# Kernel optimization log

Measured on AMD Instinct MI355X. Metric: run time of the kernel, lower is better.

## Reference

```python
import jax, jax.numpy as jnp
import numpy as np

N_NODES = 100000
N_EDGES = 3200000
N_FEAT = 512
HIDDEN = 16
OUT_DIM = 1


def setup_inputs() -> dict:
    key = jax.random.key(0)
    ks = jax.random.split(key, 6)
    x = jax.random.normal(ks[0], (N_NODES, N_FEAT), dtype=jnp.float32)
    lap_vals = jax.random.uniform(ks[1], (N_EDGES,), dtype=jnp.float32)
    W1 = jax.random.normal(ks[2], (N_FEAT, HIDDEN), dtype=jnp.float32) * 0.05
    b1 = jnp.zeros((HIDDEN,), dtype=jnp.float32)
    W2 = jax.random.normal(ks[3], (HIDDEN, OUT_DIM), dtype=jnp.float32) * 0.05
    b2 = jnp.zeros((OUT_DIM,), dtype=jnp.float32)
    lap_rows = jax.random.randint(ks[4], (N_EDGES,), 0, N_NODES, dtype=jnp.int32)
    lap_cols = jax.random.randint(ks[5], (N_EDGES,), 0, N_NODES, dtype=jnp.int32)
    return {"x": x, "lap_vals": lap_vals, "W1": W1, "b1": b1,
            "W2": W2, "b2": b2, "lap_rows": lap_rows, "lap_cols": lap_cols}


def _spmm(vals, rows, cols, dense):
    # COO sparse [N,N] @ dense [N,D]: gather source rows, scale, scatter-add.
    return jax.ops.segment_sum(vals[:, None] * dense[cols], rows,
                               num_segments=N_NODES)


def reference(x, lap_vals, W1, b1, W2, b2, lap_rows, lap_cols):
    # Layer 1: dense GEMM -> sparse aggregation -> fused bias + relu
    h = jax.nn.relu(_spmm(lap_vals, lap_rows, lap_cols, x @ W1) + b1)
    # Layer 2: dense GEMM -> sparse aggregation -> fused bias + sigmoid
    out = jax.nn.sigmoid(_spmm(lap_vals, lap_rows, lap_cols, h @ W2) + b2)
    return out
```

## Files before the change

### kernel.cpp

```cpp
#include <hip/hip_runtime.h>
#include <cstdint>
#include <cstddef>

#define N_NODES 100000
#define N_EDGES 3200000
#define N_FEAT  512
#define HIDDEN  16
#define NBUCK   ((N_NODES + 127) / 128)
#define BCAP    4608
#define CHUNK   2048
#define NGB     ((N_NODES + 63) / 64)
#define NBS     ((N_EDGES + CHUNK - 1) / CHUNK)
#define AGG_T   512

static_assert(NGB == NBS, "parity interleave requires equal role counts");

__device__ __forceinline__ void gload_lds16(const float* g, void* lds) {
  __builtin_amdgcn_global_load_lds(
      (const __attribute__((address_space(1))) void*)g,
      (__attribute__((address_space(3))) void*)lds, 16, 0, 0);
}

__global__ __launch_bounds__(256)
void k_prep(int* __restrict__ cursor) {
  const int i = blockIdx.x * 256 + threadIdx.x;
  if (i < NBUCK) cursor[i] = 0;
}

__global__ __launch_bounds__(256)
void k_mega2(const float* __restrict__ x, const float* __restrict__ W1,
             float* __restrict__ xw, const int* __restrict__ rows,
             const int* __restrict__ cols, const float* __restrict__ vals,
             int* __restrict__ cursor, int2* __restrict__ binned) {
  __shared__ __align__(16) char smem[32768];
  const int t = threadIdx.x;

  if ((blockIdx.x & 1) == 0) {
    float4 (*xs)[2][256] = reinterpret_cast<float4 (*)[2][256]>(smem);
    const int l = t & 63;
    const int w = __builtin_amdgcn_readfirstlane(t >> 6);
    const int rbase = (blockIdx.x >> 1) * 64;
    const int kbase0 = w * 128;

    float acc[16];
#pragma unroll
    for (int c = 0; c < 16; ++c) acc[c] = 0.f;

    const int sq   = ((l & 3) ^ ((l >> 3) & 3)) * 4;
    const int srow = l >> 2;

    auto STAGE = [&](int b, int ck) {
      const int kb = kbase0 + ck * 16;
#pragma unroll
      for (int i = 0; i < 4; ++i) {
        int grow = rbase + i * 16 + srow;
        if (grow >= N_NODES) grow = N_NODES - 1;
        gload_lds16(x + (size_t)grow * N_FEAT + kb + sq, &xs[w][b][i * 64]);
      }
    };

    const int rsw = (l >> 1) & 3;
    auto COMPUTE = [&](int b, int ck) {
      const int kb = kbase0 + ck * 16;
#pragma unroll
      for (int q = 0; q < 4; ++q) {
        float4 xv = xs[w][b][l * 4 + (q ^ rsw)];
        float xe[4] = {xv.x, xv.y, xv.z, xv.w};
#pragma unroll
        for (int j = 0; j < 4; ++j) {
          const float* wrow = W1 + (size_t)(kb + q * 4 + j) * 16;
#pragma unroll
          for (int c = 0; c < 16; ++c)
            acc[c] = fmaf(xe[j], wrow[c], acc[c]);
        }
      }
    };

    STAGE(0, 0);
#pragma unroll 1
    for (int ck = 0; ck < 8; ++ck) {
      const int b = ck & 1;
      if (ck + 1 < 8) {
        STAGE(b ^ 1, ck + 1);
        asm volatile("s_waitcnt vmcnt(4)" ::: "memory");
      } else {
        asm volatile("s_waitcnt vmcnt(0)" ::: "memory");
      }
      COMPUTE(b, ck);
    }

    float4* red = &xs[w][0][0];
    red[l * 4 + 0] = make_float4(acc[0],  acc[1],  acc[2],  acc[3]);
    red[l * 4 + 1] = make_float4(acc[4],  acc[5],  acc[6],  acc[7]);
    red[l * 4 + 2] = make_float4(acc[8],  acc[9],  acc[10], acc[11]);
    red[l * 4 + 3] = make_float4(acc[12], acc[13], acc[14], acc[15]);
    __syncthreads();

    const int rr = t >> 2, qq = t & 3;
    const int grow = rbase + rr;
    if (grow < N_NODES) {
      const int s = rr * 4 + qq;
      float4 a = xs[0][0][s], b4 = xs[1][0][s], c4 = xs[2][0][s], d4 = xs[3][0][s];
      float4 o = make_float4(a.x + b4.x + c4.x + d4.x, a.y + b4.y + c4.y + d4.y,
                             a.z + b4.z + c4.z + d4.z, a.w + b4.w + c4.w + d4.w);
      ((float4*)xw)[(size_t)grow * 4 + qq] = o;
    }
  } else {
    int2*           stash = (int2*)smem;
    unsigned short* sbuck = (unsigned short*)(smem + 16384);
    int*            hist  = (int*)(smem + 16384 + 4096);
    int*            base  = (int*)(smem + 16384 + 4096 + 4 * NBUCK);
    const int e0 = (blockIdx.x >> 1) * CHUNK;
    const int nv = (N_EDGES - e0 < CHUNK) ? (N_EDGES - e0) : CHUNK;

    for (int b = t; b < NBUCK; b += 256) hist[b] = 0;
    __syncthreads();

#pragma unroll
    for (int i = 0; i < CHUNK / 256; ++i) {
      const int idx = i * 256 + t;
      if (idx < nv) {
        const int e = e0 + idx;
        const int r = rows[e], c = cols[e];
        const float v = vals[e];
        const int b = r >> 7;
        stash[idx] = make_int2(c | ((r & 127) << 20), __float_as_int(v));
        sbuck[idx] = (unsigned short)b;
        atomicAdd(&hist[b], 1);
      }
    }
    __syncthreads();

    for (int b = t; b < NBUCK; b += 256) {
      const int h = hist[b];
      base[b] = (h > 0) ? atomicAdd(&cursor[b], h) : 0;
      hist[b] = 0;
    }
    __syncthreads();

#pragma unroll
    for (int i = 0; i < CHUNK / 256; ++i) {
      const int idx = i * 256 + t;
      if (idx < nv) {
        const int b = sbuck[idx];
        const int off = base[b] + atomicAdd(&hist[b], 1);
        if (off < BCAP) binned[(size_t)b * BCAP + off] = stash[idx];
      }
    }
  }
}

__global__ __launch_bounds__(AGG_T)
void k_sortagg(const int2* __restrict__ binned, const int* __restrict__ cursor,
               int2* __restrict__ binned2, int* __restrict__ row_beg,
               int* __restrict__ row_end, const float* __restrict__ xw,
               const float* __restrict__ b1, const float* __restrict__ W2,
               float* __restrict__ hw1) {
  __shared__ int2 stash[BCAP];
  __shared__ int hist[128];
  __shared__ int inc[128];
  __shared__ int cnt2[128];
  const int t = threadIdx.x;
  const int b = blockIdx.x;
  const int raw = cursor[b];
  const int cnt = raw < BCAP ? raw : BCAP;
  const int2* ep = binned + (size_t)b * BCAP;

  if (t < 128) { hist[t] = 0; cnt2[t] = 0; }
  __syncthreads();

  for (int i = t; i < cnt; i += AGG_T)
    atomicAdd(&hist[(ep[i].x >> 20) & 127], 1);
  __syncthreads();

  if (t < 128) inc[t] = hist[t];
  __syncthreads();
#pragma unroll
  for (int off = 1; off < 128; off <<= 1) {
    int add = (t >= off && t < 128) ? inc[t - off] : 0;
    __syncthreads();
    if (t < 128) inc[t] += add;
    __syncthreads();
  }

  if (t < 128) {
    const int r = b * 128 + t;
    if (r < N_NODES) {
      row_beg[r] = b * BCAP + inc[t] - hist[t];
      row_end[r] = b * BCAP + inc[t];
    }
  }

  for (int i = t; i < cnt; i += AGG_T) {
    const int2 e = ep[i];
    const int row = (e.x >> 20) & 127;
    const int off = inc[row] - hist[row] + atomicAdd(&cnt2[row], 1);
    stash[off] = e;
  }
  __syncthreads();

  int2* eq = binned2 + (size_t)b * BCAP;
  for (int i = t; i < cnt; i += AGG_T) eq[i] = stash[i];

  const int lane16 = t & 15;
  const int g = t >> 4;
  const float bb = b1[lane16];
  const float ww = W2[lane16];
#pragma unroll 1
  for (int rr = g; rr < 128; rr += 32) {
    const int r = b * 128 + rr;
    if (r >= N_NODES) continue;
    const int s = inc[rr] - hist[rr], e2 = inc[rr];
    float a0 = 0.f, a1 = 0.f, a2 = 0.f, a3 = 0.f;
    int i = s;
    for (; i + 3 < e2; i += 4) {
      int2 ea = stash[i],     eb = stash[i + 1];
      int2 ec = stash[i + 2], ed = stash[i + 3];
      a0 = fmaf(__int_as_float(ea.y), xw[(size_t)(ea.x & 0xFFFFF) * 16 + lane16], a0);
      a1 = fmaf(__int_as_float(eb.y), xw[(size_t)(eb.x & 0xFFFFF) * 16 + lane16], a1);
      a2 = fmaf(__int_as_float(ec.y), xw[(size_t)(ec.x & 0xFFFFF) * 16 + lane16], a2);
      a3 = fmaf(__int_as_float(ed.y), xw[(size_t)(ed.x & 0xFFFFF) * 16 + lane16], a3);
    }
    for (; i < e2; ++i) {
      int2 ea = stash[i];
      a0 = fmaf(__int_as_float(ea.y), xw[(size_t)(ea.x & 0xFFFFF) * 16 + lane16], a0);
    }
    float h = fmaxf((a0 + a1) + (a2 + a3) + bb, 0.f);
    float p = h * ww;
#pragma unroll
    for (int m = 8; m >= 1; m >>= 1) p += __shfl_xor(p, m, 16);
    if (lane16 == 0) hw1[r] = p;
  }
}

__global__ __launch_bounds__(256)
void k_fused2(const int2* __restrict__ binned2, const int* __restrict__ row_beg,
              const int* __restrict__ row_end, const float* __restrict__ hw1,
              const float* __restrict__ b2, float* __restrict__ out) {
  const int t = threadIdx.x;
  const int lane16 = t & 15;
  const int r = blockIdx.x * 16 + (t >> 4);
  if (r >= N_NODES) return;
  const int s = row_beg[r], e = row_end[r];
  float acc = 0.f;
  for (int i = s + lane16; i < e; i += 16) {
    int2 ev = binned2[i];
    acc = fmaf(__int_as_float(ev.y), hw1[ev.x & 0xFFFFF], acc);
  }
#pragma unroll
  for (int m = 8; m >= 1; m >>= 1) acc += __shfl_xor(acc, m, 16);
  if (lane16 == 0) out[r] = 1.f / (1.f + expf(-(acc + b2[0])));
}

extern "C" void kernel_launch(void* const* d_in, const int* in_sizes, int n_in,
                              void* d_out, int out_size, void* d_ws, size_t ws_size,
                              hipStream_t stream) {
  const float* x    = (const float*)d_in[0];
  const float* vals = (const float*)d_in[1];
  const float* W1   = (const float*)d_in[2];
  const float* b1   = (const float*)d_in[3];
  const float* W2   = (const float*)d_in[4];
  const float* b2   = (const float*)d_in[5];
  const int*   rows = (const int*)d_in[6];
  const int*   cols = (const int*)d_in[7];
  float* out = (float*)d_out;

  char* w = (char*)d_ws;
  float* xw      = (float*)w;  w += (size_t)N_NODES * 16 * 4;
  int2*  binned  = (int2*)w;   w += (size_t)NBUCK * BCAP * 8;
  int2*  binned2 = (int2*)w;   w += (size_t)NBUCK * BCAP * 8;
  int*   cursor  = (int*)w;    w += (size_t)((NBUCK + 3) & ~3) * 4;
  int*   row_beg = (int*)w;    w += (size_t)N_NODES * 4;
  int*   row_end = (int*)w;    w += (size_t)N_NODES * 4;
  float* hw1     = (float*)w;

  k_prep    <<<(NBUCK + 255) / 256, 256,   0, stream>>>(cursor);
  k_mega2   <<<NGB + NBS,           256,   0, stream>>>(x, W1, xw, rows, cols,
                                                        vals, cursor, binned);
  k_sortagg <<<NBUCK,               AGG_T, 0, stream>>>(binned, cursor, binned2,
                                                        row_beg, row_end, xw,
                                                        b1, W2, hw1);
  k_fused2  <<<(N_NODES + 15) / 16, 256,   0, stream>>>(binned2, row_beg, row_end,
                                                        hw1, b2, out);
}
```

Baseline: 155.5 us.

## Restructure fused GEMM/binscatter kernel: thread-per-row GEMM, smaller LDS, mod-5 role interleave

Replaces the LDS-staged, wave-split GEMM (four waves splitting K, then an LDS reduction) with one thread per node row that streams its 512 features straight from global memory with register double-buffering. The binscatter role drops its LDS stash and re-reads rows, cols and vals from global in the scatter pass, which shrinks shared memory to just the histogram. Blocks now use a 1:4 GEMM:binscatter interleave with launch bounds that ask for 6 blocks per CU. The aim is higher occupancy and less LDS and sync overhead. In exchange, per-thread row loads are strided and uncoalesced across lanes, and the edge arrays are read twice.

```diff
diff --git a/kernel.cpp b/kernel.cpp
--- a/kernel.cpp
+++ b/kernel.cpp
@@ -9,17 +9,11 @@
 #define NBUCK   ((N_NODES + 127) / 128)
 #define BCAP    4608
 #define CHUNK   2048
-#define NGB     ((N_NODES + 63) / 64)
+#define NGB     ((N_NODES + 255) / 256)
 #define NBS     ((N_EDGES + CHUNK - 1) / CHUNK)
 #define AGG_T   512
 
-static_assert(NGB == NBS, "parity interleave requires equal role counts");
-
-__device__ __forceinline__ void gload_lds16(const float* g, void* lds) {
-  __builtin_amdgcn_global_load_lds(
-      (const __attribute__((address_space(1))) void*)g,
-      (__attribute__((address_space(3))) void*)lds, 16, 0, 0);
-}
+static_assert(4 * NGB >= NBS, "mod-5 interleave must cover all binscatter blocks");
 
 __global__ __launch_bounds__(256)
 void k_prep(int* __restrict__ cursor) {
@@ -27,125 +21,87 @@
   if (i < NBUCK) cursor[i] = 0;
 }
 
-__global__ __launch_bounds__(256)
-void k_mega2(const float* __restrict__ x, const float* __restrict__ W1,
+__global__ __launch_bounds__(256, 6)
+void k_mega4(const float* __restrict__ x, const float* __restrict__ W1,
              float* __restrict__ xw, const int* __restrict__ rows,
              const int* __restrict__ cols, const float* __restrict__ vals,
              int* __restrict__ cursor, int2* __restrict__ binned) {
-  __shared__ __align__(16) char smem[32768];
+  __shared__ int hist[NBUCK];
   const int t = threadIdx.x;
-
-  if ((blockIdx.x & 1) == 0) {
-    float4 (*xs)[2][256] = reinterpret_cast<float4 (*)[2][256]>(smem);
-    const int l = t & 63;
-    const int w = __builtin_amdgcn_readfirstlane(t >> 6);
-    const int rbase = (blockIdx.x >> 1) * 64;
-    const int kbase0 = w * 128;
+  const int role = blockIdx.x % 5;
+
+  if (role == 0) {
+    const int gid  = blockIdx.x / 5;
+    const int rrow = gid * 256 + t;
+    const int grow = rrow < N_NODES ? rrow : N_NODES - 1;
+    const float* __restrict__ xr = x + (size_t)grow * N_FEAT;
 
     float acc[16];
 #pragma unroll
     for (int c = 0; c < 16; ++c) acc[c] = 0.f;
 
-    const int sq   = ((l & 3) ^ ((l >> 3) & 3)) * 4;
-    const int srow = l >> 2;
-
-    auto STAGE = [&](int b, int ck) {
-      const int kb = kbase0 + ck * 16;
-#pragma unroll
-      for (int i = 0; i < 4; ++i) {
-        int grow = rbase + i * 16 + srow;
-        if (grow >= N_NODES) grow = N_NODES - 1;
-        gload_lds16(x + (size_t)grow * N_FEAT + kb + sq, &xs[w][b][i * 64]);
+    float4 c0 = *(const float4*)(xr + 0);
+    float4 c1 = *(const float4*)(xr + 4);
+    float4 c2 = *(const float4*)(xr + 8);
+    float4 c3 = *(const float4*)(xr + 12);
+
+#pragma unroll 1
+    for (int ck = 0; ck < 32; ++ck) {
+      const int kb = ck * 16;
+      float4 n0 = c0, n1 = c1, n2 = c2, n3 = c3;
+      if (ck + 1 < 32) {
+        const float* p = xr + kb + 16;
+        n0 = *(const float4*)(p + 0);
+        n1 = *(const float4*)(p + 4);
+        n2 = *(const float4*)(p + 8);
+        n3 = *(const float4*)(p + 12);
       }
-    };
-
-    const int rsw = (l >> 1) & 3;
-    auto COMPUTE = [&](int b, int ck) {
-      const int kb = kbase0 + ck * 16;
-#pragma unroll
-      for (int q = 0; q < 4; ++q) {
-        float4 xv = xs[w][b][l * 4 + (q ^ rsw)];
-        float xe[4] = {xv.x, xv.y, xv.z, xv.w};
-#pragma unroll
-        for (int j = 0; j < 4; ++j) {
-          const float* wrow = W1 + (size_t)(kb + q * 4 + j) * 16;
-#pragma unroll
-          for (int c = 0; c < 16; ++c)
-            acc[c] = fmaf(xe[j], wrow[c], acc[c]);
-        }
+      const float xe[16] = {c0.x, c0.y, c0.z, c0.w,  c1.x, c1.y, c1.z, c1.w,
+                            c2.x, c2.y, c2.z, c2.w,  c3.x, c3.y, c3.z, c3.w};
+#pragma unroll
+      for (int j = 0; j < 16; ++j) {
+        const float* wrow = W1 + (size_t)(kb + j) * 16;
+#pragma unroll
+        for (int c = 0; c < 16; ++c)
+          acc[c] = fmaf(xe[j], wrow[c], acc[c]);
       }
-    };
-
-    STAGE(0, 0);
-#pragma unroll 1
-    for (int ck = 0; ck < 8; ++ck) {
-      const int b = ck & 1;
-      if (ck + 1 < 8) {
-        STAGE(b ^ 1, ck + 1);
-        asm volatile("s_waitcnt vmcnt(4)" ::: "memory");
-      } else {
-        asm volatile("s_waitcnt vmcnt(0)" ::: "memory");
-      }
-      COMPUTE(b, ck);
-    }
-
-    float4* red = &xs[w][0][0];
-    red[l * 4 + 0] = make_float4(acc[0],  acc[1],  acc[2],  acc[3]);
-    red[l * 4 + 1] = make_float4(acc[4],  acc[5],  acc[6],  acc[7]);
-    red[l * 4 + 2] = make_float4(acc[8],  acc[9],  acc[10], acc[11]);
-    red[l * 4 + 3] = make_float4(acc[12], acc[13], acc[14], acc[15]);
-    __syncthreads();
-
-    const int rr = t >> 2, qq = t & 3;
-    const int grow = rbase + rr;
-    if (grow < N_NODES) {
-      const int s = rr * 4 + qq;
-      float4 a = xs[0][0][s], b4 = xs[1][0][s], c4 = xs[2][0][s], d4 = xs[3][0][s];
-      float4 o = make_float4(a.x + b4.x + c4.x + d4.x, a.y + b4.y + c4.y + d4.y,
-                             a.z + b4.z + c4.z + d4.z, a.w + b4.w + c4.w + d4.w);
-      ((float4*)xw)[(size_t)grow * 4 + qq] = o;
+      c0 = n0; c1 = n1; c2 = n2; c3 = n3;
+    }
+
+    if (rrow < N_NODES) {
+      float4* o = (float4*)(xw + (size_t)rrow * 16);
+      o[0] = make_float4(acc[0],  acc[1],  acc[2],  acc[3]);
+      o[1] = make_float4(acc[4],  acc[5],  acc[6],  acc[7]);
+      o[2] = make_float4(acc[8],  acc[9],  acc[10], acc[11]);
+      o[3] = make_float4(acc[12], acc[13], acc[14], acc[15]);
     }
   } else {
-    int2*           stash = (int2*)smem;
-    unsigned short* sbuck = (unsigned short*)(smem + 16384);
-    int*            hist  = (int*)(smem + 16384 + 4096);
-    int*            base  = (int*)(smem + 16384 + 4096 + 4 * NBUCK);
-    const int e0 = (blockIdx.x >> 1) * CHUNK;
+    const int bsid = (blockIdx.x / 5) * 4 + role - 1;
+    if (bsid >= NBS) return;
+    const int e0 = bsid * CHUNK;
     const int nv = (N_EDGES - e0 < CHUNK) ? (N_EDGES - e0) : CHUNK;
 
     for (int b = t; b < NBUCK; b += 256) hist[b] = 0;
     __syncthreads();
 
-#pragma unroll
-    for (int i = 0; i < CHUNK / 256; ++i) {
-      const int idx = i * 256 + t;
-      if (idx < nv) {
-        const int e = e0 + idx;
-        const int r = rows[e], c = cols[e];
-        const float v = vals[e];
-        const int b = r >> 7;
-        stash[idx] = make_int2(c | ((r & 127) << 20), __float_as_int(v));
-        sbuck[idx] = (unsigned short)b;
-        atomicAdd(&hist[b], 1);
-      }
-    }
+    for (int i = t; i < nv; i += 256)
+      atomicAdd(&hist[rows[e0 + i] >> 7], 1);
     __syncthreads();
 
     for (int b = t; b < NBUCK; b += 256) {
       const int h = hist[b];
-      base[b] = (h > 0) ? atomicAdd(&cursor[b], h) : 0;
-      hist[b] = 0;
-    }
-    __syncthreads();
-
-#pragma unroll
-    for (int i = 0; i < CHUNK / 256; ++i) {
-      const int idx = i * 256 + t;
-      if (idx < nv) {
-        const int b = sbuck[idx];
-        const int off = base[b] + atomicAdd(&hist[b], 1);
-        if (off < BCAP) binned[(size_t)b * BCAP + off] = stash[idx];
-      }
+      hist[b] = (h > 0) ? atomicAdd(&cursor[b], h) : 0;
+    }
+    __syncthreads();
+
+    for (int i = t; i < nv; i += 256) {
+      const int e = e0 + i;
+      const int r = rows[e];
+      const int b = r >> 7;
+      const int off = atomicAdd(&hist[b], 1);
+      if (off < BCAP)
+        binned[(size_t)b * BCAP + off] =
+            make_int2(cols[e] | ((r & 127) << 20), __float_as_int(vals[e]));
     }
   }
 }
@@ -275,7 +231,7 @@
   float* hw1     = (float*)w;
 
   k_prep    <<<(NBUCK + 255) / 256, 256,   0, stream>>>(cursor);
-  k_mega2   <<<NGB + NBS,           256,   0, stream>>>(x, W1, xw, rows, cols,
+  k_mega4   <<<5 * NGB,             256,   0, stream>>>(x, W1, xw, rows, cols,
                                                         vals, cursor, binned);
   k_sortagg <<<NBUCK,               AGG_T, 0, stream>>>(binned, cursor, binned2,
                                                         row_beg, row_end, xw,
```

Measured after the change: 238.7 us. +53.5%, slower.

## Halve LDS in fused GEMM/binning kernel via register prefetch and re-read edges

Applied to the files above, without the earlier changes.

The GEMM role drops the double-buffered direct-to-LDS loads in favour of register prefetch into a single LDS buffer, written after each compute step. The binning role no longer stashes edges and bucket ids in LDS; it re-reads rows from global memory for the second pass and reuses the histogram array as the running offset. Together these cut shared memory per block from 32 KB to 16 KB, aiming for higher occupancy. The cost is extra global reads of rows, cols and vals, more register pressure for the prefetch, and an LDS read-after-write ordering in the GEMM path that has no barrier.

```diff
diff --git a/kernel.cpp b/kernel.cpp
--- a/kernel.cpp
+++ b/kernel.cpp
@@ -15,12 +15,6 @@
 
 static_assert(NGB == NBS, "parity interleave requires equal role counts");
 
-__device__ __forceinline__ void gload_lds16(const float* g, void* lds) {
-  __builtin_amdgcn_global_load_lds(
-      (const __attribute__((address_space(1))) void*)g,
-      (__attribute__((address_space(3))) void*)lds, 16, 0, 0);
-}
-
 __global__ __launch_bounds__(256)
 void k_prep(int* __restrict__ cursor) {
   const int i = blockIdx.x * 256 + threadIdx.x;
@@ -28,15 +22,15 @@
 }
 
 __global__ __launch_bounds__(256)
-void k_mega2(const float* __restrict__ x, const float* __restrict__ W1,
+void k_mega5(const float* __restrict__ x, const float* __restrict__ W1,
              float* __restrict__ xw, const int* __restrict__ rows,
              const int* __restrict__ cols, const float* __restrict__ vals,
              int* __restrict__ cursor, int2* __restrict__ binned) {
-  __shared__ __align__(16) char smem[32768];
+  __shared__ __align__(16) char smem[16384];
   const int t = threadIdx.x;
 
   if ((blockIdx.x & 1) == 0) {
-    float4 (*xs)[2][256] = reinterpret_cast<float4 (*)[2][256]>(smem);
+    float4 (*xs)[256] = reinterpret_cast<float4 (*)[256]>(smem);
     const int l = t & 63;
     const int w = __builtin_amdgcn_readfirstlane(t >> 6);
     const int rbase = (blockIdx.x >> 1) * 64;
@@ -49,22 +43,27 @@
     const int sq   = ((l & 3) ^ ((l >> 3) & 3)) * 4;
     const int srow = l >> 2;
 
-    auto STAGE = [&](int b, int ck) {
+    float4 pf[4];
+    auto LOAD = [&](int ck) {
       const int kb = kbase0 + ck * 16;
 #pragma unroll
       for (int i = 0; i < 4; ++i) {
         int grow = rbase + i * 16 + srow;
         if (grow >= N_NODES) grow = N_NODES - 1;
-        gload_lds16(x + (size_t)grow * N_FEAT + kb + sq, &xs[w][b][i * 64]);
+        pf[i] = *(const float4*)(x + (size_t)grow * N_FEAT + kb + sq);
       }
     };
+    auto WRITE = [&]() {
+#pragma unroll
+      for (int i = 0; i < 4; ++i) xs[w][i * 64 + l] = pf[i];
+    };
 
     const int rsw = (l >> 1) & 3;
-    auto COMPUTE = [&](int b, int ck) {
+    auto COMPUTE = [&](int ck) {
       const int kb = kbase0 + ck * 16;
 #pragma unroll
       for (int q = 0; q < 4; ++q) {
-        float4 xv = xs[w][b][l * 4 + (q ^ rsw)];
+        float4 xv = xs[w][l * 4 + (q ^ rsw)];
         float xe[4] = {xv.x, xv.y, xv.z, xv.w};
 #pragma unroll
         for (int j = 0; j < 4; ++j) {
@@ -76,20 +75,18 @@
       }
     };
 
-    STAGE(0, 0);
+    LOAD(0); WRITE();
+    LOAD(1);
 #pragma unroll 1
     for (int ck = 0; ck < 8; ++ck) {
-      const int b = ck & 1;
+      COMPUTE(ck);
       if (ck + 1 < 8) {
-        STAGE(b ^ 1, ck + 1);
-        asm volatile("s_waitcnt vmcnt(4)" ::: "memory");
-      } else {
-        asm volatile("s_waitcnt vmcnt(0)" ::: "memory");
+        WRITE();
+        if (ck + 2 < 8) LOAD(ck + 2);
       }
-      COMPUTE(b, ck);
-    }
-
-    float4* red = &xs[w][0][0];
+    }
+
+    float4* red = &xs[w][0];
     red[l * 4 + 0] = make_float4(acc[0],  acc[1],  acc[2],  acc[3]);
     red[l * 4 + 1] = make_float4(acc[4],  acc[5],  acc[6],  acc[7]);
     red[l * 4 + 2] = make_float4(acc[8],  acc[9],  acc[10], acc[11]);
@@ -100,52 +97,37 @@
     const int grow = rbase + rr;
     if (grow < N_NODES) {
       const int s = rr * 4 + qq;
-      float4 a = xs[0][0][s], b4 = xs[1][0][s], c4 = xs[2][0][s], d4 = xs[3][0][s];
+      float4 a = xs[0][s], b4 = xs[1][s], c4 = xs[2][s], d4 = xs[3][s];
       float4 o = make_float4(a.x + b4.x + c4.x + d4.x, a.y + b4.y + c4.y + d4.y,
                              a.z + b4.z + c4.z + d4.z, a.w + b4.w + c4.w + d4.w);
       ((float4*)xw)[(size_t)grow * 4 + qq] = o;
     }
   } else {
-    int2*           stash = (int2*)smem;
-    unsigned short* sbuck = (unsigned short*)(smem + 16384);
-    int*            hist  = (int*)(smem + 16384 + 4096);
-    int*            base  = (int*)(smem + 16384 + 4096 + 4 * NBUCK);
+    int* hist = (int*)smem;
     const int e0 = (blockIdx.x >> 1) * CHUNK;
     const int nv = (N_EDGES - e0 < CHUNK) ? (N_EDGES - e0) : CHUNK;
 
     for (int b = t; b < NBUCK; b += 256) hist[b] = 0;
     __syncthreads();
 
-#pragma unroll
-    for (int i = 0; i < CHUNK / 256; ++i) {
-      const int idx = i * 256 + t;
-      if (idx < nv) {
-        const int e = e0 + idx;
-        const int r = rows[e], c = cols[e];
-        const float v = vals[e];
-        const int b = r >> 7;
-        stash[idx] = make_int2(c | ((r & 127) << 20), __float_as_int(v));
-        sbuck[idx] = (unsigned short)b;
-        atomicAdd(&hist[b], 1);
-      }
-    }
+    for (int i = t; i < nv; i += 256)
+      atomicAdd(&hist[rows[e0 + i] >> 7], 1);
     __syncthreads();
 
     for (int b = t; b < NBUCK; b += 256) {
       const int h = hist[b];
-      base[b] = (h > 0) ? atomicAdd(&cursor[b], h) : 0;
-      hist[b] = 0;
-    }
-    __syncthreads();
-
-#pragma unroll
-    for (int i = 0; i < CHUNK / 256; ++i) {
-      const int idx = i * 256 + t;
-      if (idx < nv) {
-        const int b = sbuck[idx];
-        const int off = base[b] + atomicAdd(&hist[b], 1);
-        if (off < BCAP) binned[(size_t)b * BCAP + off] = stash[idx];
-      }
+      hist[b] = (h > 0) ? atomicAdd(&cursor[b], h) : 0;
+    }
+    __syncthreads();
+
+    for (int i = t; i < nv; i += 256) {
+      const int e = e0 + i;
+      const int r = rows[e];
+      const int b = r >> 7;
+      const int off = atomicAdd(&hist[b], 1);
+      if (off < BCAP)
+        binned[(size_t)b * BCAP + off] =
+            make_int2(cols[e] | ((r & 127) << 20), __float_as_int(vals[e]));
     }
   }
 }
@@ -275,7 +257,7 @@
   float* hw1     = (float*)w;
 
   k_prep    <<<(NBUCK + 255) / 256, 256,   0, stream>>>(cursor);
-  k_mega2   <<<NGB + NBS,           256,   0, stream>>>(x, W1, xw, rows, cols,
+  k_mega5   <<<NGB + NBS,           256,   0, stream>>>(x, W1, xw, rows, cols,
                                                         vals, cursor, binned);
   k_sortagg <<<NBUCK,               AGG_T, 0, stream>>>(binned, cursor, binned2,
                                                         row_beg, row_end, xw,
```

Result: slower. 268.6 us (+72.8%).
